# Optimization experiments

Hardware: AMD Instinct MI355X
Metric: run time of the kernel (lower is better)

## Reference

```python
import jax, jax.numpy as jnp
import numpy as np

N_QUBITS = 4
N_QLAYERS = 2
B = 524288


def setup_inputs() -> dict:
    key = jax.random.key(0)
    ks = jax.random.split(key, 12)
    s = 0.1
    return {
        "x": jax.random.normal(ks[0], (B, 2), jnp.float32),
        "enc_w1": jax.random.normal(ks[1], (2, 64), jnp.float32) * s,
        "enc_b1": jnp.zeros((64,), jnp.float32),
        "enc_w2": jax.random.normal(ks[2], (64, 16), jnp.float32) * s,
        "enc_b2": jnp.zeros((16,), jnp.float32),
        "pre_w": jax.random.normal(ks[3], (16, N_QUBITS), jnp.float32) * s,
        "pre_b": jnp.zeros((N_QUBITS,), jnp.float32),
        "q_weights": jax.random.uniform(ks[4], (N_QLAYERS, N_QUBITS), jnp.float32, 0.0, 2.0 * np.pi),
        "post_w1": jax.random.normal(ks[5], (N_QUBITS, 32), jnp.float32) * s,
        "post_b1": jnp.zeros((32,), jnp.float32),
        "post_w2": jax.random.normal(ks[6], (32, 4), jnp.float32) * s,
        "post_b2": jnp.zeros((4,), jnp.float32),
    }


def _ry(state, theta, q):
    # state: [B,2,2,2,2] real statevector; theta: scalar or [B]
    c, sn = jnp.cos(theta / 2), jnp.sin(theta / 2)
    if jnp.ndim(c) == 1:  # per-sample angle (embedding)
        c = c[:, None, None, None]
        sn = sn[:, None, None, None]
    st = jnp.moveaxis(state, q + 1, -1)
    new = jnp.stack([c * st[..., 0] - sn * st[..., 1],
                     sn * st[..., 0] + c * st[..., 1]], axis=-1)
    return jnp.moveaxis(new, -1, q + 1)


def _cnot(state, ctrl, tgt):
    st = jnp.moveaxis(state, (ctrl + 1, tgt + 1), (-2, -1))
    st = jnp.concatenate([st[..., 0:1, :], st[..., 1:2, ::-1]], axis=-2)
    return jnp.moveaxis(st, (-2, -1), (ctrl + 1, tgt + 1))


def q_layer(q_in, q_weights):
    # batched 4-qubit circuit: RY embedding + BasicEntanglerLayers, <Z_i> readout
    b = q_in.shape[0]
    state = jnp.zeros((b, 2 ** N_QUBITS), q_in.dtype).at[:, 0].set(1.0)
    state = state.reshape((b,) + (2,) * N_QUBITS)
    for q in range(N_QUBITS):
        state = _ry(state, q_in[:, q], q)
    for l in range(N_QLAYERS):
        for q in range(N_QUBITS):
            state = _ry(state, q_weights[l, q], q)
        for c_, t_ in [(0, 1), (1, 2), (2, 3), (3, 0)]:
            state = _cnot(state, c_, t_)
    probs = state * state  # real amplitudes -> probabilities
    exps = []
    for q in range(N_QUBITS):
        axes = tuple(a for a in range(1, N_QUBITS + 1) if a != q + 1)
        marg = probs.sum(axes)  # [B,2]
        exps.append(marg[:, 0] - marg[:, 1])
    return jnp.stack(exps, axis=-1)  # [B,4]


def reference(x, enc_w1, enc_b1, enc_w2, enc_b2, pre_w, pre_b, q_weights,
              post_w1, post_b1, post_w2, post_b2):
    z = jnp.tanh(x @ enc_w1 + enc_b1)
    z = jnp.tanh(z @ enc_w2 + enc_b2)
    q_in = z @ pre_w + pre_b
    q_out = q_layer(q_in, q_weights)
    h = jnp.tanh(q_out @ post_w1 + post_b1)
    return h @ post_w2 + post_b2
```

## Files before the change

### kernel.cpp

```cpp
#include <hip/hip_runtime.h>
#include <math.h>

#define NQ 4

typedef _Float16 f16;
typedef _Float16 f16x8 __attribute__((ext_vector_type(8)));
typedef __fp16 fp16x2 __attribute__((ext_vector_type(2)));
typedef float f32x4 __attribute__((ext_vector_type(4)));
typedef float v2f __attribute__((ext_vector_type(2)));

#define K_TANH 2.885390081777927f
#define BETA2  0.15915494309189535f

__device__ __forceinline__ v2f b2(float s) { v2f r; r.x = s; r.y = s; return r; }

__device__ __forceinline__ v2f tanh4v(v2f a) {
    v2f e;
    e.x = __builtin_amdgcn_exp2f(a.x);
    e.y = __builtin_amdgcn_exp2f(a.y);
    v2f d = e + 1.0f;
    v2f r;
    r.x = __builtin_amdgcn_rcpf(d.x);
    r.y = __builtin_amdgcn_rcpf(d.y);
    return __builtin_elementwise_fma(b2(-2.0f), r, b2(1.0f));
}
__device__ __forceinline__ v2f tanh5v(v2f a) {
    return tanh4v(a * K_TANH);
}

union U8 { f16x8 v8; fp16x2 v2[4]; };

__shared__ float z2s[256][20];
__shared__ float cpre[12];

extern "C" __global__ void __launch_bounds__(256)
hybrid_pinn_kernel(const float* __restrict__ x,
                   const float* __restrict__ ew1, const float* __restrict__ eb1,
                   const float* __restrict__ ew2, const float* __restrict__ eb2,
                   const float* __restrict__ pw,  const float* __restrict__ pb,
                   const float* __restrict__ qw,
                   const float* __restrict__ pw1, const float* __restrict__ pb1,
                   const float* __restrict__ pw2, const float* __restrict__ pb2,
                   float* __restrict__ out)
{
    const int tid   = threadIdx.x;
    const int lane  = tid & 63;
    const int wbase = (tid >> 6) * 64;
    const int brow0 = blockIdx.x * 256;
    const int ak    = (lane >> 4) * 8;
    const int bn    = lane & 15;

    if (tid < 4) {
        float s, c;
        __sincosf(qw[4 + tid], &s, &c);
        cpre[tid] = c; cpre[4 + tid] = s;
        cpre[8 + tid] = qw[tid] * BETA2;
    }
    __syncthreads();

    U8 bf0, bf1;
#pragma unroll
    for (int p = 0; p < 4; ++p) {
        v2f w0, w1;
        w0.x = ew2[(ak + 2 * p) * 16 + bn];
        w0.y = ew2[(ak + 2 * p + 1) * 16 + bn];
        w1.x = ew2[(32 + ak + 2 * p) * 16 + bn];
        w1.y = ew2[(32 + ak + 2 * p + 1) * 16 + bn];
        w0 = w0 * K_TANH;
        w1 = w1 * K_TANH;
        bf0.v2[p] = __builtin_amdgcn_cvt_pkrtz(w0.x, w0.y);
        bf1.v2[p] = __builtin_amdgcn_cvt_pkrtz(w1.x, w1.y);
    }

    const float2* x2 = reinterpret_cast<const float2*>(x);
    float2 xr[4];
#pragma unroll
    for (int mt = 0; mt < 4; ++mt)
        xr[mt] = x2[brow0 + wbase + (lane & 15) + mt * 16];

    f16x8 afrag[4][2];
#pragma unroll
    for (int kt = 0; kt < 2; ++kt) {
        const int base = kt * 32 + ak;
        v2f w0[4], w1[4], bb[4];
#pragma unroll
        for (int p = 0; p < 4; ++p) {
            w0[p] = *reinterpret_cast<const v2f*>(&ew1[base + 2 * p]) * K_TANH;
            w1[p] = *reinterpret_cast<const v2f*>(&ew1[64 + base + 2 * p]) * K_TANH;
            bb[p] = *reinterpret_cast<const v2f*>(&eb1[base + 2 * p]) * K_TANH;
        }
#pragma unroll
        for (int mt = 0; mt < 4; ++mt) {
            U8 u;
#pragma unroll
            for (int p = 0; p < 4; ++p) {
                v2f a = __builtin_elementwise_fma(
                            b2(xr[mt].y), w1[p],
                            __builtin_elementwise_fma(b2(xr[mt].x), w0[p], bb[p]));
                v2f t = tanh4v(a);
                u.v2[p] = __builtin_amdgcn_cvt_pkrtz(t.x, t.y);
            }
            afrag[mt][kt] = u.v8;
        }
    }

    const float ebc = eb2[bn] * K_TANH;
    f32x4 acc[4];
#pragma unroll
    for (int mt = 0; mt < 4; ++mt) {
        f32x4 z = {ebc, ebc, ebc, ebc};
        z = __builtin_amdgcn_mfma_f32_16x16x32_f16(afrag[mt][0], bf0.v8, z, 0, 0, 0);
        z = __builtin_amdgcn_mfma_f32_16x16x32_f16(afrag[mt][1], bf1.v8, z, 0, 0, 0);
        acc[mt] = z;
    }
#pragma unroll
    for (int mt = 0; mt < 4; ++mt) {
#pragma unroll
        for (int j = 0; j < 4; ++j)
            z2s[wbase + mt * 16 + (lane >> 4) * 4 + j][bn] = acc[mt][j];
    }

    float z2[16];
    {
        float4 r0 = *reinterpret_cast<const float4*>(&z2s[tid][0]);
        float4 r1 = *reinterpret_cast<const float4*>(&z2s[tid][4]);
        float4 r2 = *reinterpret_cast<const float4*>(&z2s[tid][8]);
        float4 r3 = *reinterpret_cast<const float4*>(&z2s[tid][12]);
        z2[0]=r0.x; z2[1]=r0.y; z2[2]=r0.z; z2[3]=r0.w;
        z2[4]=r1.x; z2[5]=r1.y; z2[6]=r1.z; z2[7]=r1.w;
        z2[8]=r2.x; z2[9]=r2.y; z2[10]=r2.z; z2[11]=r2.w;
        z2[12]=r3.x; z2[13]=r3.y; z2[14]=r3.z; z2[15]=r3.w;
    }
#pragma unroll
    for (int j = 0; j < 8; ++j) {
        v2f t; t.x = z2[2 * j]; t.y = z2[2 * j + 1];
        t = tanh4v(t);
        z2[2 * j] = t.x; z2[2 * j + 1] = t.y;
    }

    v2f tq01 = *reinterpret_cast<const v2f*>(&pb[0]);
    v2f tq23 = *reinterpret_cast<const v2f*>(&pb[2]);
#pragma unroll
    for (int i = 0; i < 16; ++i) {
        v2f zi = b2(z2[i]);
        tq01 = __builtin_elementwise_fma(zi, *reinterpret_cast<const v2f*>(&pw[i * 4]),     tq01);
        tq23 = __builtin_elementwise_fma(zi, *reinterpret_cast<const v2f*>(&pw[i * 4 + 2]), tq23);
    }

    float C0, C1, C2, C3, S0, S1, S2, S3;
    {
        float t0 = __builtin_amdgcn_fractf(fmaf(tq01.x, BETA2, cpre[8]));
        float t1 = __builtin_amdgcn_fractf(fmaf(tq01.y, BETA2, cpre[9]));
        float t2 = __builtin_amdgcn_fractf(fmaf(tq23.x, BETA2, cpre[10]));
        float t3 = __builtin_amdgcn_fractf(fmaf(tq23.y, BETA2, cpre[11]));
        S0 = __builtin_amdgcn_sinf(t0); C0 = __builtin_amdgcn_cosf(t0);
        S1 = __builtin_amdgcn_sinf(t1); C1 = __builtin_amdgcn_cosf(t1);
        S2 = __builtin_amdgcn_sinf(t2); C2 = __builtin_amdgcn_cosf(t2);
        S3 = __builtin_amdgcn_sinf(t3); C3 = __builtin_amdgcn_cosf(t3);
    }

    const float c0 = cpre[0], c1 = cpre[1], c2 = cpre[2], c3 = cpre[3];
    const float s0 = cpre[4], s1 = cpre[5], s2 = cpre[6], s3 = cpre[7];
    const float c12 = c1 * c2, s12 = s1 * s2, sc12 = s1 * c2, cs12 = c1 * s2;
    const float A1 = c12 * c3,  A2 = c12 * s3,  A3 = sc12 * c3, A4 = s12 * s3;
    const float B1 = c0 * c1,   B2 = s0 * s1;
    const float D1 = c0 * c12,  D2 = c0 * sc12, D3 = s0 * c12,  D4 = s0 * s12;
    const float c0s12 = c0 * s12, s0s12 = s0 * s12;
    const float E1 = D1 * c3,          E2 = (c0 * cs12) * c3;
    const float E3 = c0s12 * c3,       E4 = D3 * s3;
    const float E5 = (s0 * sc12) * c3, E6 = c0s12 * s3;
    const float E7 = (s0 * cs12) * s3, E8 = s0s12 * s3;

    const float C01 = C0 * C1, C13 = C1 * C3, C02 = C0 * C2, C23 = C2 * C3;
    const float S01 = S0 * S1, S02 = S0 * S2, S12 = S1 * S2, S13 = S1 * S3;
    const float S23 = S2 * S3, C2S3 = C2 * S3;

    float qo[NQ];
    qo[0] = A1 * (C0 * C13) - A2 * (S01 * C2S3) - A3 * (S12 * C3) - A4 * S0;
    qo[1] = B1 * (C02 * C3) + B2 * S02;
    qo[2] = D1 * C13 - D2 * ((C0 * S12) * C3) - D3 * (S01 * C2) - D4 * (S0 * S3);
    qo[3] = E1 * C02 - E2 * (C1 * S23) + E3 * (C0 * S13) + E4 * C2S3
          + E5 * (S02 * C3) - E6 * ((S0 * C1) * C23) - E7 * (C01 * S2) + E8 * S1;

    float h[32];
#pragma unroll
    for (int j = 0; j < 16; ++j) {
        v2f a = *reinterpret_cast<const v2f*>(&pb1[2 * j]);
#pragma unroll
        for (int i = 0; i < NQ; ++i)
            a = __builtin_elementwise_fma(b2(qo[i]),
                    *reinterpret_cast<const v2f*>(&pw1[i * 32 + 2 * j]), a);
        v2f t = tanh5v(a);
        h[2 * j]     = t.x;
        h[2 * j + 1] = t.y;
    }

    v2f o01 = *reinterpret_cast<const v2f*>(&pb2[0]);
    v2f o23 = *reinterpret_cast<const v2f*>(&pb2[2]);
#pragma unroll
    for (int i = 0; i < 32; ++i) {
        v2f hi = b2(h[i]);
        o01 = __builtin_elementwise_fma(hi, *reinterpret_cast<const v2f*>(&pw2[i * 4]),     o01);
        o23 = __builtin_elementwise_fma(hi, *reinterpret_cast<const v2f*>(&pw2[i * 4 + 2]), o23);
    }

    reinterpret_cast<float4*>(out)[brow0 + tid] = make_float4(o01.x, o01.y, o23.x, o23.y);
}

extern "C" void kernel_launch(void* const* d_in, const int* in_sizes, int n_in,
                              void* d_out, int out_size, void* d_ws, size_t ws_size,
                              hipStream_t stream) {
    const float* x   = (const float*)d_in[0];
    const float* ew1 = (const float*)d_in[1];
    const float* eb1 = (const float*)d_in[2];
    const float* ew2 = (const float*)d_in[3];
    const float* eb2 = (const float*)d_in[4];
    const float* pw  = (const float*)d_in[5];
    const float* pb  = (const float*)d_in[6];
    const float* qw  = (const float*)d_in[7];
    const float* pw1 = (const float*)d_in[8];
    const float* pb1 = (const float*)d_in[9];
    const float* pw2 = (const float*)d_in[10];
    const float* pb2 = (const float*)d_in[11];
    float* out = (float*)d_out;

    const int rows = in_sizes[0] / 2;
    hipLaunchKernelGGL(hybrid_pinn_kernel, dim3(rows / 256), dim3(256), 0, stream,
                       x, ew1, eb1, ew2, eb2, pw, pb, qw,
                       pw1, pb1, pw2, pb2, out);
}
```

Baseline: 23.77 us.

## Process two row tiles per block and precompute circuit constants in shared memory

Each block now handles two 256-row tiles in a grid-strided loop, with the grid halved. The per-block prologue (ew2 MFMA fragment setup, eb2 load, quantum constants) is paid once per two tiles instead of once per tile. Thread 0 now computes all the trigonometric products of the fixed layer weights into shared memory, and the main body reads them as float4 vectors, which removes per-thread scalar constant arithmetic. The cost is fewer blocks to hide latency, possible extra register pressure from the unrolled loop, and a longer serial prologue on one thread before the barrier.

```diff
diff --git a/kernel.cpp b/kernel.cpp
--- a/kernel.cpp
+++ b/kernel.cpp
@@ -30,8 +30,8 @@
 
 union U8 { f16x8 v8; fp16x2 v2[4]; };
 
-__shared__ float z2s[256][20];
-__shared__ float cpre[12];
+__shared__ __align__(16) float z2s[256][20];
+__shared__ __align__(16) float cpre[24];
 
 extern "C" __global__ void __launch_bounds__(256)
 hybrid_pinn_kernel(const float* __restrict__ x,
@@ -46,15 +46,40 @@
     const int tid   = threadIdx.x;
     const int lane  = tid & 63;
     const int wbase = (tid >> 6) * 64;
-    const int brow0 = blockIdx.x * 256;
     const int ak    = (lane >> 4) * 8;
     const int bn    = lane & 15;
 
-    if (tid < 4) {
-        float s, c;
-        __sincosf(qw[4 + tid], &s, &c);
-        cpre[tid] = c; cpre[4 + tid] = s;
-        cpre[8 + tid] = qw[tid] * BETA2;
+    if (tid == 0) {
+        float c0, c1, c2, c3, s0, s1, s2, s3;
+        __sincosf(qw[4], &s0, &c0);
+        __sincosf(qw[5], &s1, &c1);
+        __sincosf(qw[6], &s2, &c2);
+        __sincosf(qw[7], &s3, &c3);
+        const float c12 = c1 * c2, s12 = s1 * s2, sc12 = s1 * c2, cs12 = c1 * s2;
+        const float c0s12 = c0 * s12, s0s12 = s0 * s12;
+        cpre[0]  = c12 * c3;
+        cpre[1]  = c12 * s3;
+        cpre[2]  = sc12 * c3;
+        cpre[3]  = s12 * s3;
+        cpre[4]  = c0 * c1;
+        cpre[5]  = s0 * s1;
+        cpre[6]  = c0 * c12;
+        cpre[7]  = c0 * sc12;
+        cpre[8]  = s0 * c12;
+        cpre[9]  = s0s12;
+        cpre[10] = (c0 * c12) * c3;
+        cpre[11] = (c0 * cs12) * c3;
+        cpre[12] = c0s12 * c3;
+        cpre[13] = (s0 * c12) * s3;
+        cpre[14] = (s0 * sc12) * c3;
+        cpre[15] = c0s12 * s3;
+        cpre[16] = (s0 * cs12) * s3;
+        cpre[17] = s0s12 * s3;
+        cpre[18] = 0.0f; cpre[19] = 0.0f;
+        cpre[20] = qw[0] * BETA2;
+        cpre[21] = qw[1] * BETA2;
+        cpre[22] = qw[2] * BETA2;
+        cpre[23] = qw[3] * BETA2;
     }
     __syncthreads();
 
@@ -71,140 +96,141 @@
         bf0.v2[p] = __builtin_amdgcn_cvt_pkrtz(w0.x, w0.y);
         bf1.v2[p] = __builtin_amdgcn_cvt_pkrtz(w1.x, w1.y);
     }
+    const float ebc = eb2[bn] * K_TANH;
 
     const float2* x2 = reinterpret_cast<const float2*>(x);
-    float2 xr[4];
-#pragma unroll
-    for (int mt = 0; mt < 4; ++mt)
-        xr[mt] = x2[brow0 + wbase + (lane & 15) + mt * 16];
-
-    f16x8 afrag[4][2];
-#pragma unroll
-    for (int kt = 0; kt < 2; ++kt) {
-        const int base = kt * 32 + ak;
-        v2f w0[4], w1[4], bb[4];
-#pragma unroll
-        for (int p = 0; p < 4; ++p) {
-            w0[p] = *reinterpret_cast<const v2f*>(&ew1[base + 2 * p]) * K_TANH;
-            w1[p] = *reinterpret_cast<const v2f*>(&ew1[64 + base + 2 * p]) * K_TANH;
-            bb[p] = *reinterpret_cast<const v2f*>(&eb1[base + 2 * p]) * K_TANH;
-        }
+
+#pragma unroll
+    for (int it = 0; it < 2; ++it) {
+        const int brow0 = (blockIdx.x + it * (int)gridDim.x) * 256;
+
+        float2 xr[4];
+#pragma unroll
+        for (int mt = 0; mt < 4; ++mt)
+            xr[mt] = x2[brow0 + wbase + (lane & 15) + mt * 16];
+
+        f16x8 afrag[4][2];
+#pragma unroll
+        for (int kt = 0; kt < 2; ++kt) {
+            const int base = kt * 32 + ak;
+            v2f w0[4], w1[4], bb[4];
+#pragma unroll
+            for (int p = 0; p < 4; ++p) {
+                w0[p] = *reinterpret_cast<const v2f*>(&ew1[base + 2 * p]) * K_TANH;
+                w1[p] = *reinterpret_cast<const v2f*>(&ew1[64 + base + 2 * p]) * K_TANH;
+                bb[p] = *reinterpret_cast<const v2f*>(&eb1[base + 2 * p]) * K_TANH;
+            }
+#pragma unroll
+            for (int mt = 0; mt < 4; ++mt) {
+                U8 u;
+#pragma unroll
+                for (int p = 0; p < 4; ++p) {
+                    v2f a = __builtin_elementwise_fma(
+                                b2(xr[mt].y), w1[p],
+                                __builtin_elementwise_fma(b2(xr[mt].x), w0[p], bb[p]));
+                    v2f t = tanh4v(a);
+                    u.v2[p] = __builtin_amdgcn_cvt_pkrtz(t.x, t.y);
+                }
+                afrag[mt][kt] = u.v8;
+            }
+        }
+
+        f32x4 acc[4];
 #pragma unroll
         for (int mt = 0; mt < 4; ++mt) {
-            U8 u;
-#pragma unroll
-            for (int p = 0; p < 4; ++p) {
-                v2f a = __builtin_elementwise_fma(
-                            b2(xr[mt].y), w1[p],
-                            __builtin_elementwise_fma(b2(xr[mt].x), w0[p], bb[p]));
-                v2f t = tanh4v(a);
-                u.v2[p] = __builtin_amdgcn_cvt_pkrtz(t.x, t.y);
-            }
-            afrag[mt][kt] = u.v8;
-        }
+            f32x4 z = {ebc, ebc, ebc, ebc};
+            z = __builtin_amdgcn_mfma_f32_16x16x32_f16(afrag[mt][0], bf0.v8, z, 0, 0, 0);
+            z = __builtin_amdgcn_mfma_f32_16x16x32_f16(afrag[mt][1], bf1.v8, z, 0, 0, 0);
+            acc[mt] = z;
+        }
+#pragma unroll
+        for (int mt = 0; mt < 4; ++mt) {
+#pragma unroll
+            for (int j = 0; j < 4; ++j)
+                z2s[wbase + mt * 16 + (lane >> 4) * 4 + j][bn] = acc[mt][j];
+        }
+
+        float z2[16];
+        {
+            float4 r0 = *reinterpret_cast<const float4*>(&z2s[tid][0]);
+            float4 r1 = *reinterpret_cast<const float4*>(&z2s[tid][4]);
+            float4 r2 = *reinterpret_cast<const float4*>(&z2s[tid][8]);
+            float4 r3 = *reinterpret_cast<const float4*>(&z2s[tid][12]);
+            z2[0]=r0.x; z2[1]=r0.y; z2[2]=r0.z; z2[3]=r0.w;
+            z2[4]=r1.x; z2[5]=r1.y; z2[6]=r1.z; z2[7]=r1.w;
+            z2[8]=r2.x; z2[9]=r2.y; z2[10]=r2.z; z2[11]=r2.w;
+            z2[12]=r3.x; z2[13]=r3.y; z2[14]=r3.z; z2[15]=r3.w;
+        }
+#pragma unroll
+        for (int j = 0; j < 8; ++j) {
+            v2f t; t.x = z2[2 * j]; t.y = z2[2 * j + 1];
+            t = tanh4v(t);
+            z2[2 * j] = t.x; z2[2 * j + 1] = t.y;
+        }
+
+        v2f tq01 = *reinterpret_cast<const v2f*>(&pb[0]);
+        v2f tq23 = *reinterpret_cast<const v2f*>(&pb[2]);
+#pragma unroll
+        for (int i = 0; i < 16; ++i) {
+            v2f zi = b2(z2[i]);
+            tq01 = __builtin_elementwise_fma(zi, *reinterpret_cast<const v2f*>(&pw[i * 4]),     tq01);
+            tq23 = __builtin_elementwise_fma(zi, *reinterpret_cast<const v2f*>(&pw[i * 4 + 2]), tq23);
+        }
+
+        const float4 uq = *reinterpret_cast<const float4*>(&cpre[20]);
+        float C0, C1, C2, C3, S0, S1, S2, S3;
+        {
+            float t0 = __builtin_amdgcn_fractf(fmaf(tq01.x, BETA2, uq.x));
+            float t1 = __builtin_amdgcn_fractf(fmaf(tq01.y, BETA2, uq.y));
+            float t2 = __builtin_amdgcn_fractf(fmaf(tq23.x, BETA2, uq.z));
+            float t3 = __builtin_amdgcn_fractf(fmaf(tq23.y, BETA2, uq.w));
+            S0 = __builtin_amdgcn_sinf(t0); C0 = __builtin_amdgcn_cosf(t0);
+            S1 = __builtin_amdgcn_sinf(t1); C1 = __builtin_amdgcn_cosf(t1);
+            S2 = __builtin_amdgcn_sinf(t2); C2 = __builtin_amdgcn_cosf(t2);
+            S3 = __builtin_amdgcn_sinf(t3); C3 = __builtin_amdgcn_cosf(t3);
+        }
+
+        const float4 qA = *reinterpret_cast<const float4*>(&cpre[0]);
+        const float4 qB = *reinterpret_cast<const float4*>(&cpre[4]);
+        const float4 qC = *reinterpret_cast<const float4*>(&cpre[8]);
+        const float4 qD = *reinterpret_cast<const float4*>(&cpre[12]);
+        const float4 qE = *reinterpret_cast<const float4*>(&cpre[16]);
+
+        const float C01 = C0 * C1, C13 = C1 * C3, C02 = C0 * C2, C23 = C2 * C3;
+        const float S01 = S0 * S1, S02 = S0 * S2, S12 = S1 * S2, S13 = S1 * S3;
+        const float S23 = S2 * S3, C2S3 = C2 * S3;
+
+        float qo[NQ];
+        qo[0] = qA.x * (C0 * C13) - qA.y * (S01 * C2S3) - qA.z * (S12 * C3) - qA.w * S0;
+        qo[1] = qB.x * (C02 * C3) + qB.y * S02;
+        qo[2] = qB.z * C13 - qB.w * ((C0 * S12) * C3) - qC.x * (S01 * C2) - qC.y * (S0 * S3);
+        qo[3] = qC.z * C02 - qC.w * (C1 * S23) + qD.x * (C0 * S13) + qD.y * C2S3
+              + qD.z * (S02 * C3) - qD.w * ((S0 * C1) * C23) - qE.x * (C01 * S2) + qE.y * S1;
+
+        float h[32];
+#pragma unroll
+        for (int j = 0; j < 16; ++j) {
+            v2f a = *reinterpret_cast<const v2f*>(&pb1[2 * j]);
+#pragma unroll
+            for (int i = 0; i < NQ; ++i)
+                a = __builtin_elementwise_fma(b2(qo[i]),
+                        *reinterpret_cast<const v2f*>(&pw1[i * 32 + 2 * j]), a);
+            v2f t = tanh5v(a);
+            h[2 * j]     = t.x;
+            h[2 * j + 1] = t.y;
+        }
+
+        v2f o01 = *reinterpret_cast<const v2f*>(&pb2[0]);
+        v2f o23 = *reinterpret_cast<const v2f*>(&pb2[2]);
+#pragma unroll
+        for (int i = 0; i < 32; ++i) {
+            v2f hi = b2(h[i]);
+            o01 = __builtin_elementwise_fma(hi, *reinterpret_cast<const v2f*>(&pw2[i * 4]),     o01);
+            o23 = __builtin_elementwise_fma(hi, *reinterpret_cast<const v2f*>(&pw2[i * 4 + 2]), o23);
+        }
+
+        reinterpret_cast<float4*>(out)[brow0 + tid] = make_float4(o01.x, o01.y, o23.x, o23.y);
     }
-
-    const float ebc = eb2[bn] * K_TANH;
-    f32x4 acc[4];
-#pragma unroll
-    for (int mt = 0; mt < 4; ++mt) {
-        f32x4 z = {ebc, ebc, ebc, ebc};
-        z = __builtin_amdgcn_mfma_f32_16x16x32_f16(afrag[mt][0], bf0.v8, z, 0, 0, 0);
-        z = __builtin_amdgcn_mfma_f32_16x16x32_f16(afrag[mt][1], bf1.v8, z, 0, 0, 0);
-        acc[mt] = z;
-    }
-#pragma unroll
-    for (int mt = 0; mt < 4; ++mt) {
-#pragma unroll
-        for (int j = 0; j < 4; ++j)
-            z2s[wbase + mt * 16 + (lane >> 4) * 4 + j][bn] = acc[mt][j];
-    }
-
-    float z2[16];
-    {
-        float4 r0 = *reinterpret_cast<const float4*>(&z2s[tid][0]);
-        float4 r1 = *reinterpret_cast<const float4*>(&z2s[tid][4]);
-        float4 r2 = *reinterpret_cast<const float4*>(&z2s[tid][8]);
-        float4 r3 = *reinterpret_cast<const float4*>(&z2s[tid][12]);
-        z2[0]=r0.x; z2[1]=r0.y; z2[2]=r0.z; z2[3]=r0.w;
-        z2[4]=r1.x; z2[5]=r1.y; z2[6]=r1.z; z2[7]=r1.w;
-        z2[8]=r2.x; z2[9]=r2.y; z2[10]=r2.z; z2[11]=r2.w;
-        z2[12]=r3.x; z2[13]=r3.y; z2[14]=r3.z; z2[15]=r3.w;
-    }
-#pragma unroll
-    for (int j = 0; j < 8; ++j) {
-        v2f t; t.x = z2[2 * j]; t.y = z2[2 * j + 1];
-        t = tanh4v(t);
-        z2[2 * j] = t.x; z2[2 * j + 1] = t.y;
-    }
-
-    v2f tq01 = *reinterpret_cast<const v2f*>(&pb[0]);
-    v2f tq23 = *reinterpret_cast<const v2f*>(&pb[2]);
-#pragma unroll
-    for (int i = 0; i < 16; ++i) {
-        v2f zi = b2(z2[i]);
-        tq01 = __builtin_elementwise_fma(zi, *reinterpret_cast<const v2f*>(&pw[i * 4]),     tq01);
-        tq23 = __builtin_elementwise_fma(zi, *reinterpret_cast<const v2f*>(&pw[i * 4 + 2]), tq23);
-    }
-
-    float C0, C1, C2, C3, S0, S1, S2, S3;
-    {
-        float t0 = __builtin_amdgcn_fractf(fmaf(tq01.x, BETA2, cpre[8]));
-        float t1 = __builtin_amdgcn_fractf(fmaf(tq01.y, BETA2, cpre[9]));
-        float t2 = __builtin_amdgcn_fractf(fmaf(tq23.x, BETA2, cpre[10]));
-        float t3 = __builtin_amdgcn_fractf(fmaf(tq23.y, BETA2, cpre[11]));
-        S0 = __builtin_amdgcn_sinf(t0); C0 = __builtin_amdgcn_cosf(t0);
-        S1 = __builtin_amdgcn_sinf(t1); C1 = __builtin_amdgcn_cosf(t1);
-        S2 = __builtin_amdgcn_sinf(t2); C2 = __builtin_amdgcn_cosf(t2);
-        S3 = __builtin_amdgcn_sinf(t3); C3 = __builtin_amdgcn_cosf(t3);
-    }
-
-    const float c0 = cpre[0], c1 = cpre[1], c2 = cpre[2], c3 = cpre[3];
-    const float s0 = cpre[4], s1 = cpre[5], s2 = cpre[6], s3 = cpre[7];
-    const float c12 = c1 * c2, s12 = s1 * s2, sc12 = s1 * c2, cs12 = c1 * s2;
-    const float A1 = c12 * c3,  A2 = c12 * s3,  A3 = sc12 * c3, A4 = s12 * s3;
-    const float B1 = c0 * c1,   B2 = s0 * s1;
-    const float D1 = c0 * c12,  D2 = c0 * sc12, D3 = s0 * c12,  D4 = s0 * s12;
-    const float c0s12 = c0 * s12, s0s12 = s0 * s12;
-    const float E1 = D1 * c3,          E2 = (c0 * cs12) * c3;
-    const float E3 = c0s12 * c3,       E4 = D3 * s3;
-    const float E5 = (s0 * sc12) * c3, E6 = c0s12 * s3;
-    const float E7 = (s0 * cs12) * s3, E8 = s0s12 * s3;
-
-    const float C01 = C0 * C1, C13 = C1 * C3, C02 = C0 * C2, C23 = C2 * C3;
-    const float S01 = S0 * S1, S02 = S0 * S2, S12 = S1 * S2, S13 = S1 * S3;
-    const float S23 = S2 * S3, C2S3 = C2 * S3;
-
-    float qo[NQ];
-    qo[0] = A1 * (C0 * C13) - A2 * (S01 * C2S3) - A3 * (S12 * C3) - A4 * S0;
-    qo[1] = B1 * (C02 * C3) + B2 * S02;
-    qo[2] = D1 * C13 - D2 * ((C0 * S12) * C3) - D3 * (S01 * C2) - D4 * (S0 * S3);
-    qo[3] = E1 * C02 - E2 * (C1 * S23) + E3 * (C0 * S13) + E4 * C2S3
-          + E5 * (S02 * C3) - E6 * ((S0 * C1) * C23) - E7 * (C01 * S2) + E8 * S1;
-
-    float h[32];
-#pragma unroll
-    for (int j = 0; j < 16; ++j) {
-        v2f a = *reinterpret_cast<const v2f*>(&pb1[2 * j]);
-#pragma unroll
-        for (int i = 0; i < NQ; ++i)
-            a = __builtin_elementwise_fma(b2(qo[i]),
-                    *reinterpret_cast<const v2f*>(&pw1[i * 32 + 2 * j]), a);
-        v2f t = tanh5v(a);
-        h[2 * j]     = t.x;
-        h[2 * j + 1] = t.y;
-    }
-
-    v2f o01 = *reinterpret_cast<const v2f*>(&pb2[0]);
-    v2f o23 = *reinterpret_cast<const v2f*>(&pb2[2]);
-#pragma unroll
-    for (int i = 0; i < 32; ++i) {
-        v2f hi = b2(h[i]);
-        o01 = __builtin_elementwise_fma(hi, *reinterpret_cast<const v2f*>(&pw2[i * 4]),     o01);
-        o23 = __builtin_elementwise_fma(hi, *reinterpret_cast<const v2f*>(&pw2[i * 4 + 2]), o23);
-    }
-
-    reinterpret_cast<float4*>(out)[brow0 + tid] = make_float4(o01.x, o01.y, o23.x, o23.y);
 }
 
 extern "C" void kernel_launch(void* const* d_in, const int* in_sizes, int n_in,
@@ -225,7 +251,8 @@
     float* out = (float*)d_out;
 
     const int rows = in_sizes[0] / 2;
-    hipLaunchKernelGGL(hybrid_pinn_kernel, dim3(rows / 256), dim3(256), 0, stream,
+    const int grid = rows / 512;
+    hipLaunchKernelGGL(hybrid_pinn_kernel, dim3(grid), dim3(256), 0, stream,
                        x, ew1, eb1, ew2, eb2, pw, pb, qw,
                        pw1, pb1, pw2, pb2, out);
 }
```

After: 24.37 us. 2.5% more time.
